# Kernel tuning notes

Hardware: AMD Instinct MI355X
Metric: run time of the kernel (lower is better)

## Reference

```python
import jax, jax.numpy as jnp
from jax import lax
import numpy as np

C = 192      # dim
L = 2        # focal_level
T = 8        # num_frames
KS = (3, 5)  # kernel_size = focal_factor*k + focal_window
B, H, W = 32, 56, 56  # B = 4 clips * T frames


def _gelu(v):
    return jax.nn.gelu(v, approximate=False)  # torch nn.GELU (erf)


def _dwconv2d(x, w):
    # x: (B,C,H,W), w: (C,1,k,k) depthwise; odd k + SAME == padding k//2
    return lax.conv_general_dilated(x, w, (1, 1), 'SAME',
                                    feature_group_count=x.shape[1],
                                    dimension_numbers=('NCHW', 'OIHW', 'NCHW'))


def _conv1d(x, w):
    # x: (N,C,T), w: (Cout,Cin,k) dense conv1d, SAME padding
    return lax.conv_general_dilated(x, w, (1,), 'SAME',
                                    dimension_numbers=('NCH', 'OIH', 'NCH'))


def setup_inputs() -> dict:
    key = jax.random.key(0)
    ks = jax.random.split(key, 12)
    s = 0.02
    return {
        'x':   jax.random.normal(ks[0], (B, H, W, C), jnp.float32),
        'Wf':  jax.random.normal(ks[1], (C, 2 * C + L + 1), jnp.float32) * s,
        'bf':  jnp.zeros((2 * C + L + 1,), jnp.float32),
        'Wft': jax.random.normal(ks[2], (C, C + L + 1), jnp.float32) * s,
        'bft': jnp.zeros((C + L + 1,), jnp.float32),
        'fw0': jax.random.normal(ks[3], (C, 1, KS[0], KS[0]), jnp.float32) * s,
        'fw1': jax.random.normal(ks[4], (C, 1, KS[1], KS[1]), jnp.float32) * s,
        'tw0': jax.random.normal(ks[5], (C, C, KS[0]), jnp.float32) * s,
        'tw1': jax.random.normal(ks[6], (C, C, KS[1]), jnp.float32) * s,
        'Wh':  jax.random.normal(ks[7], (C, C), jnp.float32) * s,
        'bh':  jnp.zeros((C,), jnp.float32),
        'Wht': jax.random.normal(ks[8], (C, C), jnp.float32) * s,
        'bht': jnp.zeros((C,), jnp.float32),
        'Wp':  jax.random.normal(ks[9], (C, C), jnp.float32) * s,
        'bp':  jnp.zeros((C,), jnp.float32),
    }


def reference(x, Wf, bf, Wft, bft, fw0, fw1, tw0, tw1, Wh, bh, Wht, bht, Wp, bp):
    Bt, Hh, Ww, Cc = x.shape
    b = Bt // T
    # ---- temporal branch: (b t) h w c -> (b h w) t c
    xt = x.reshape(b, T, Hh, Ww, Cc).transpose(0, 2, 3, 1, 4).reshape(b * Hh * Ww, T, Cc)
    xt = (xt @ Wft + bft).transpose(0, 2, 1)          # (N, C+L+1, T)
    ctx_t, gates_t = xt[:, :Cc], xt[:, Cc:]
    ctx_all_t = jnp.zeros_like(ctx_t)
    for l, tw in enumerate((tw0, tw1)):
        ctx_t = _gelu(_conv1d(ctx_t, tw))
        ctx_all_t = ctx_all_t + ctx_t * gates_t[:, l:l + 1]
    ctx_all_t = ctx_all_t + _gelu(ctx_t.mean(2, keepdims=True)) * gates_t[:, L:]
    mod_t = jnp.einsum('nct,oc->not', ctx_all_t, Wht) + bht[None, :, None]  # h_temporal 1x1
    # (b h w) c t -> (b t) c h w
    mod_t = mod_t.reshape(b, Hh, Ww, Cc, T).transpose(0, 4, 3, 1, 2).reshape(Bt, Cc, Hh, Ww)
    # ---- spatial branch
    xs = (x @ Wf + bf).transpose(0, 3, 1, 2)           # (B, 2C+L+1, H, W)
    q, ctx, gates = xs[:, :Cc], xs[:, Cc:2 * Cc], xs[:, 2 * Cc:]
    ctx_all = jnp.zeros_like(ctx)
    for l, fw in enumerate((fw0, fw1)):
        ctx = _gelu(_dwconv2d(ctx, fw))
        ctx_all = ctx_all + ctx * gates[:, l:l + 1]
    ctx_all = ctx_all + _gelu(ctx.mean((2, 3), keepdims=True)) * gates[:, L:]
    mod = jnp.einsum('bchw,oc->bohw', ctx_all, Wh) + bh[None, :, None, None]  # h 1x1
    x_out = (q * mod * mod_t).transpose(0, 2, 3, 1)    # (B,H,W,C)
    return x_out @ Wp + bp
```

## Files before the change

### kernel.cpp

```cpp
#include <hip/hip_runtime.h>
#include <math.h>

#define CC    192
#define TT    8
#define HH    56
#define WWD   56
#define PP    3136
#define NTOK  100352
#define NSEQ  12544

typedef __attribute__((ext_vector_type(8))) short short8v;
typedef __attribute__((ext_vector_type(4))) float f32x4;
using u16 = unsigned short;

__device__ __forceinline__ float gelu_f(float v) {
  return 0.5f * v * (1.0f + erff(v * 0.70710678f));
}

__device__ __forceinline__ u16 bf16hi(float f) {
  unsigned u = __builtin_bit_cast(unsigned, f);
  u += 0x7fffu + ((u >> 16) & 1u);
  return (u16)(u >> 16);
}
__device__ __forceinline__ float bf2f(u16 h) {
  unsigned u = ((unsigned)h) << 16;
  return __builtin_bit_cast(float, u);
}

__device__ __forceinline__ void split4(float4 v, uint2* ph, uint2* pl) {
  float vv[4] = {v.x, v.y, v.z, v.w};
  u16 hh[4], ll[4];
  #pragma unroll
  for (int u = 0; u < 4; ++u) {
    hh[u] = bf16hi(vv[u]);
    ll[u] = bf16hi(vv[u] - bf2f(hh[u]));
  }
  *ph = make_uint2((unsigned)hh[0] | ((unsigned)hh[1] << 16),
                   (unsigned)hh[2] | ((unsigned)hh[3] << 16));
  *pl = make_uint2((unsigned)ll[0] | ((unsigned)ll[1] << 16),
                   (unsigned)ll[2] | ((unsigned)ll[3] << 16));
}

__global__ __launch_bounds__(256) void k_wsplit(const float* __restrict__ in,
    u16* __restrict__ hi, u16* __restrict__ lo, int K) {
  int idx = blockIdx.x * 256 + threadIdx.x;
  int total = CC * CC * K;
  if (idx >= total) return;
  int i = idx % CC;
  int rest = idx / CC;
  int o = rest % CC;
  int k = rest / CC;
  float f = in[(o * CC + i) * K + k];
  u16 h = bf16hi(f);
  hi[idx] = h;
  lo[idx] = bf16hi(f - bf2f(h));
}

__global__ __launch_bounds__(256) void k_wsplit_in(const float* __restrict__ Wf,
    const float* __restrict__ Wft, u16* __restrict__ hi, u16* __restrict__ lo) {
  int idx = blockIdx.x * 256 + threadIdx.x;
  if (idx >= 768 * CC) return;
  int k = idx % CC;
  int j = idx / CC;
  float f = 0.0f;
  if (j < 387) f = Wf[k * 387 + j];
  else if (j < 582) f = Wft[k * 195 + (j - 387)];
  u16 h = bf16hi(f);
  hi[idx] = h;
  lo[idx] = bf16hi(f - bf2f(h));
}

__global__ __launch_bounds__(256) void k_wsplit_d(const float* __restrict__ in,
    u16* __restrict__ hi, u16* __restrict__ lo) {
  int idx = blockIdx.x * 256 + threadIdx.x;
  if (idx >= CC * CC) return;
  float f = in[idx];
  u16 h = bf16hi(f);
  hi[idx] = h;
  lo[idx] = bf16hi(f - bf2f(h));
}

__global__ __launch_bounds__(256) void k_wsplit_t(const float* __restrict__ in,
    u16* __restrict__ hi, u16* __restrict__ lo) {
  int idx = blockIdx.x * 256 + threadIdx.x;
  if (idx >= CC * CC) return;
  int c = idx % CC;
  int o = idx / CC;
  float f = in[c * CC + o];
  u16 h = bf16hi(f);
  hi[idx] = h;
  lo[idx] = bf16hi(f - bf2f(h));
}

__global__ __launch_bounds__(256, 3) void k_in_mfma(const float* __restrict__ x,
    const u16* __restrict__ WIh, const u16* __restrict__ WIl,
    const float* __restrict__ bf, const float* __restrict__ bft,
    float* __restrict__ QS, float* __restrict__ CS, float* __restrict__ GS,
    float* __restrict__ CT, float* __restrict__ GT)
{
  __shared__ __align__(16) u16 xh[32 * 200];
  __shared__ __align__(16) u16 xl[32 * 200];
  const int tid  = threadIdx.x;
  const int lane = tid & 63;
  const int w    = tid >> 6;
  const int lrow = lane & 15;
  const int lk   = (lane >> 4) * 8;
  const int orow = (lane >> 4) * 4;
  const int tk0  = blockIdx.x * 32;
  const int jw0  = blockIdx.y * 320 + w * 80;

  #pragma unroll
  for (int it = 0; it < 6; ++it) {
    int idx = tid + it * 256;
    int tokl = idx / 48;
    int c = (idx - tokl * 48) * 4;
    float4 v = *(const float4*)(x + (size_t)(tk0 + tokl) * CC + c);
    split4(v, (uint2*)&xh[tokl * 200 + c], (uint2*)&xl[tokl * 200 + c]);
  }
  __syncthreads();

  f32x4 acc[5][2] = {};
  #pragma unroll
  for (int kb = 0; kb < 6; ++kb) {
    int k0 = kb * 32;
    short8v ah[5], al[5], bh[2], bl[2];
    #pragma unroll
    for (int r = 0; r < 5; ++r) {
      size_t aoff = (size_t)(jw0 + r * 16 + lrow) * 192 + k0 + lk;
      ah[r] = *(const short8v*)(WIh + aoff);
      al[r] = *(const short8v*)(WIl + aoff);
    }
    #pragma unroll
    for (int c = 0; c < 2; ++c) {
      int tokl = c * 16 + lrow;
      bh[c] = *(const short8v*)&xh[tokl * 200 + k0 + lk];
      bl[c] = *(const short8v*)&xl[tokl * 200 + k0 + lk];
    }
    #pragma unroll
    for (int r = 0; r < 5; ++r)
      #pragma unroll
      for (int c = 0; c < 2; ++c) {
        acc[r][c] = __builtin_amdgcn_mfma_f32_16x16x32_bf16(ah[r], bh[c], acc[r][c], 0, 0, 0);
        acc[r][c] = __builtin_amdgcn_mfma_f32_16x16x32_bf16(ah[r], bl[c], acc[r][c], 0, 0, 0);
        acc[r][c] = __builtin_amdgcn_mfma_f32_16x16x32_bf16(al[r], bh[c], acc[r][c], 0, 0, 0);
      }
  }

  #pragma unroll
  for (int c = 0; c < 2; ++c) {
    int tok = tk0 + c * 16 + lrow;
    int bb = tok / PP;
    int hw = tok - bb * PP;
    size_t ctbase = ((size_t)((bb >> 3) * PP + hw) * 8 + (size_t)(bb & 7));
    #pragma unroll
    for (int r = 0; r < 5; ++r) {
      int jb = jw0 + r * 16 + orow;
      #pragma unroll
      for (int u = 0; u < 4; ++u) {
        int j = jb + u;
        if (j >= 582) continue;
        float bias = (j < 387) ? bf[j] : bft[j - 387];
        float val = acc[r][c][u] + bias;
        if (j < 192)      QS[(size_t)tok * CC + j] = val;
        else if (j < 384) CS[(size_t)tok * CC + (j - 192)] = val;
        else if (j < 387) GS[(size_t)tok * 3 + (j - 384)] = val;
        else if (j < 579) CT[ctbase * CC + (j - 387)] = val;
        else              GT[ctbase * 3 + (j - 579)] = val;
      }
    }
  }
}

#define PADB 200
__global__ __launch_bounds__(256, 3) void k_t_mfma(
    const float* __restrict__ CT, const float* __restrict__ GT,
    const u16* __restrict__ W3h,
    const u16* __restrict__ W5h,
    const u16* __restrict__ WHh, const u16* __restrict__ WHl,
    const float* __restrict__ bht, float* __restrict__ MT)
{
  __shared__ __align__(16) u16 bufh[48 * PADB];
  __shared__ __align__(16) u16 bufl[48 * PADB];
  __shared__ float gbuf[96];

  const int tid  = threadIdx.x;
  const int lane = tid & 63;
  const int w    = tid >> 6;
  const int m0   = w * 48;
  const int lrow = lane & 15;
  const int lk   = (lane >> 4) * 8;
  const int orow = (lane >> 4) * 4;
  const int n0   = blockIdx.x * 4;

  if (tid < 96) gbuf[tid] = GT[(size_t)n0 * 24 + tid];

  for (int i = tid; i < 16 * 96; i += 256) {
    int hc = i / 96, j = i - hc * 96;
    int s = hc >> 2, which = hc & 3;
    int pc = s * 12 + ((which < 2) ? which : (8 + which));
    ((unsigned*)&bufh[pc * PADB])[j] = 0u;
    ((unsigned*)&bufl[pc * PADB])[j] = 0u;
  }

  {
    const float4* src = (const float4*)(CT + (size_t)n0 * 1536);
    #pragma unroll
    for (int it = 0; it < 6; ++it) {
      int idx = tid + it * 256;
      int e = idx * 4;
      int s = e / 1536;
      int r2 = e - s * 1536;
      int t = r2 / 192;
      int c = r2 - t * 192;
      float4 v = src[idx];
      int pc = s * 12 + 2 + t;
      split4(v, (uint2*)&bufh[pc * PADB + c], (uint2*)&bufl[pc * PADB + c]);
    }
  }
  __syncthreads();

  int pcolBase[2];
  #pragma unroll
  for (int c = 0; c < 2; ++c) {
    int col = c * 16 + lrow;
    pcolBase[c] = (col >> 3) * 12 + 2 + (col & 7);
  }

#define LOADA1(WH, OFF, KB, AH) { \
    _Pragma("unroll") for (int r = 0; r < 3; ++r) { \
      size_t aoff = ((size_t)((OFF) * 192 + m0 + r * 16 + lrow)) * 192 + (KB) * 32 + lk; \
      AH[r] = *(const short8v*)(WH + aoff); } }
#define LOADB_T(SH, KB, BH, BL) { \
    _Pragma("unroll") for (int c = 0; c < 2; ++c) { \
      int pc = pcolBase[c] + (SH); \
      BH[c] = *(const short8v*)&bufh[pc * PADB + (KB) * 32 + lk]; \
      BL[c] = *(const short8v*)&bufl[pc * PADB + (KB) * 32 + lk]; } }
#define MFMA4(AH, BH, BL, ACC) { \
    _Pragma("unroll") for (int r = 0; r < 3; ++r) \
      _Pragma("unroll") for (int c = 0; c < 2; ++c) { \
        ACC[r][c] = __builtin_amdgcn_mfma_f32_16x16x32_bf16(AH[r], BH[c], ACC[r][c], 0, 0, 0); \
        ACC[r][c] = __builtin_amdgcn_mfma_f32_16x16x32_bf16(AH[r], BL[c], ACC[r][c], 0, 0, 0); } }

  f32x4 acc[3][2] = {};
  #pragma unroll
  for (int off = 0; off < 3; ++off) {
    #pragma unroll
    for (int kb = 0; kb < 6; ++kb) {
      short8v ah[3], bh[2], bl[2];
      LOADA1(W3h, off, kb, ah);
      LOADB_T(off - 1, kb, bh, bl);
      MFMA4(ah, bh, bl, acc);
    }
  }
  __syncthreads();

  #pragma unroll
  for (int r = 0; r < 3; ++r) {
    int o = m0 + r * 16 + orow;
    #pragma unroll
    for (int c = 0; c < 2; ++c) {
      int pc = pcolBase[c];
      f32x4 a = acc[r][c];
      u16 hh[4], ll[4];
      #pragma unroll
      for (int u = 0; u < 4; ++u) {
        float c1v = gelu_f(a[u]);
        hh[u] = bf16hi(c1v);
        ll[u] = bf16hi(c1v - bf2f(hh[u]));
      }
      *(uint2*)&bufh[pc * PADB + o] =
          make_uint2((unsigned)hh[0] | ((unsigned)hh[1] << 16),
                     (unsigned)hh[2] | ((unsigned)hh[3] << 16));
      *(uint2*)&bufl[pc * PADB + o] =
          make_uint2((unsigned)ll[0] | ((unsigned)ll[1] << 16),
                     (unsigned)ll[2] | ((unsigned)ll[3] << 16));
    }
  }
  __syncthreads();

  f32x4 acc2[3][2] = {};
  #pragma unroll
  for (int off = 0; off < 5; ++off) {
    #pragma unroll
    for (int kb = 0; kb < 6; ++kb) {
      short8v ah[3], bh[2], bl[2];
      LOADA1(W5h, off, kb, ah);
      LOADB_T(off - 2, kb, bh, bl);
      MFMA4(ah, bh, bl, acc2);
    }
  }
  __syncthreads();

  #pragma unroll
  for (int r = 0; r < 3; ++r) {
    int o = m0 + r * 16 + orow;
    #pragma unroll
    for (int c = 0; c < 2; ++c) {
      int col = c * 16 + lrow;
      int pc = pcolBase[c];
      float g0 = gbuf[col * 3 + 0];
      float g1 = gbuf[col * 3 + 1];
      float g2 = gbuf[col * 3 + 2];
      f32x4 a = acc2[r][c];
      uint2 c1hv = *(const uint2*)&bufh[pc * PADB + o];
      uint2 c1lv = *(const uint2*)&bufl[pc * PADB + o];
      u16 c1h4[4] = {(u16)(c1hv.x & 0xffff), (u16)(c1hv.x >> 16),
                     (u16)(c1hv.y & 0xffff), (u16)(c1hv.y >> 16)};
      u16 c1l4[4] = {(u16)(c1lv.x & 0xffff), (u16)(c1lv.x >> 16),
                     (u16)(c1lv.y & 0xffff), (u16)(c1lv.y >> 16)};
      u16 hh[4], ll[4];
      #pragma unroll
      for (int u = 0; u < 4; ++u) {
        float cv = gelu_f(a[u]);
        float sm = cv;
        sm += __shfl_xor(sm, 1);
        sm += __shfl_xor(sm, 2);
        sm += __shfl_xor(sm, 4);
        float gm = gelu_f(sm * 0.125f);
        float c1full = bf2f(c1h4[u]) + bf2f(c1l4[u]);
        float av = c1full * g0 + cv * g1 + gm * g2;
        hh[u] = bf16hi(av);
        ll[u] = bf16hi(av - bf2f(hh[u]));
      }
      *(uint2*)&bufh[pc * PADB + o] =
          make_uint2((unsigned)hh[0] | ((unsigned)hh[1] << 16),
                     (unsigned)hh[2] | ((unsigned)hh[3] << 16));
      *(uint2*)&bufl[pc * PADB + o] =
          make_uint2((unsigned)ll[0] | ((unsigned)ll[1] << 16),
                     (unsigned)ll[2] | ((unsigned)ll[3] << 16));
    }
  }
  __syncthreads();

  f32x4 acc3[3][2] = {};
  #pragma unroll
  for (int kb = 0; kb < 6; ++kb) {
    short8v ah[3], al[3], bh[2], bl[2];
    #pragma unroll
    for (int r = 0; r < 3; ++r) {
      size_t aoff = ((size_t)(m0 + r * 16 + lrow)) * 192 + kb * 32 + lk;
      ah[r] = *(const short8v*)(WHh + aoff);
      al[r] = *(const short8v*)(WHl + aoff);
    }
    LOADB_T(0, kb, bh, bl);
    #pragma unroll
    for (int r = 0; r < 3; ++r)
      #pragma unroll
      for (int c = 0; c < 2; ++c) {
        acc3[r][c] = __builtin_amdgcn_mfma_f32_16x16x32_bf16(ah[r], bh[c], acc3[r][c], 0, 0, 0);
        acc3[r][c] = __builtin_amdgcn_mfma_f32_16x16x32_bf16(ah[r], bl[c], acc3[r][c], 0, 0, 0);
        acc3[r][c] = __builtin_amdgcn_mfma_f32_16x16x32_bf16(al[r], bh[c], acc3[r][c], 0, 0, 0);
      }
  }
#undef LOADA1
#undef LOADB_T
#undef MFMA4

  #pragma unroll
  for (int r = 0; r < 3; ++r) {
    int o = m0 + r * 16 + orow;
    float4 bb4 = *(const float4*)&bht[o];
    #pragma unroll
    for (int c = 0; c < 2; ++c) {
      int col = c * 16 + lrow;
      int n = n0 + (col >> 3);
      int t = col & 7;
      int bg = n / PP;
      int hw = n - bg * PP;
      size_t tk = (size_t)(bg * 8 + t) * PP + hw;
      f32x4 a = acc3[r][c];
      *(float4*)&MT[tk * CC + o] =
          make_float4(a[0] + bb4.x, a[1] + bb4.y, a[2] + bb4.z, a[3] + bb4.w);
    }
  }
}

__global__ __launch_bounds__(256) void k_dwf(const float* __restrict__ CTX,
    const float* __restrict__ GS, const float* __restrict__ fw0,
    const float* __restrict__ fw1, float* __restrict__ A0,
    float* __restrict__ GMpart)
{
  __shared__ __align__(16) float sctx[14 * 14 * 32];
  __shared__ __align__(16) float sc1[12 * 12 * 32];
  __shared__ float w3s[9 * 32];
  __shared__ float w5s[25 * 32];
  __shared__ float smean[256];
  const int tid  = threadIdx.x;
  const int tile = blockIdx.x;
  const int cgi  = blockIdx.y;
  const int bb   = blockIdx.z;
  const int ty0  = (tile / 7) * 8;
  const int tx0  = (tile % 7) * 8;
  const int c0   = cgi * 32;

  for (int i = tid; i < 288; i += 256) {
    int k = i / 32, c = i - (i / 32) * 32;
    w3s[k * 32 + c] = fw0[(c0 + c) * 9 + k];
  }
  for (int i = tid; i < 800; i += 256) {
    int k = i / 32, c = i - (i / 32) * 32;
    w5s[k * 32 + c] = fw1[(c0 + c) * 25 + k];
  }

  for (int i = tid; i < 1568; i += 256) {
    int tok = i >> 3;
    int part = i & 7;
    int y = tok / 14, x = tok - y * 14;
    int gh = ty0 + y - 3, gw = tx0 + x - 3;
    float4 v = make_float4(0.f, 0.f, 0.f, 0.f);
    if (gh >= 0 && gh < HH && gw >= 0 && gw < WWD)
      v = *(const float4*)(CTX + ((size_t)bb * PP + gh * WWD + gw) * CC + c0 + part * 4);
    *(float4*)&sctx[tok * 32 + part * 4] = v;
  }
  __syncthreads();

  for (int i = tid; i < 4608; i += 256) {
    int c = i & 31, tok = i >> 5;
    int y = tok / 12, x = tok - y * 12;
    float s = 0.f;
    #pragma unroll
    for (int dy = 0; dy < 3; ++dy)
      #pragma unroll
      for (int dx = 0; dx < 3; ++dx)
        s = fmaf(sctx[((y + dy) * 14 + (x + dx)) * 32 + c], w3s[(dy * 3 + dx) * 32 + c], s);
    sc1[tok * 32 + c] = gelu_f(s);
  }
  __syncthreads();

  float ms = 0.f;
  #pragma unroll
  for (int p = 0; p < 8; ++p) {
    int i = tid + p * 256;
    int c = i & 31, tok = i >> 5;
    int y = tok >> 3, x = tok & 7;
    float s = 0.f;
    #pragma unroll
    for (int dy = 0; dy < 5; ++dy)
      #pragma unroll
      for (int dx = 0; dx < 5; ++dx)
        s = fmaf(sc1[((y + dy) * 12 + (x + dx)) * 32 + c], w5s[(dy * 5 + dx) * 32 + c], s);
    float c2 = gelu_f(s);
    ms += c2;
    float c1v = sc1[((y + 2) * 12 + (x + 2)) * 32 + c];
    size_t tg = (size_t)bb * PP + (size_t)(ty0 + y) * WWD + (tx0 + x);
    float g0 = GS[tg * 3 + 0];
    float g1 = GS[tg * 3 + 1];
    A0[tg * CC + c0 + c] = c1v * g0 + c2 * g1;
  }
  smean[tid] = ms;
  __syncthreads();
  if (tid < 32) {
    float s = 0.f;
    #pragma unroll
    for (int p = 0; p < 8; ++p) s += smean[p * 32 + tid];
    GMpart[(size_t)tile * 6144 + bb * CC + c0 + tid] = s;
  }
}

__global__ __launch_bounds__(256) void k_gmg(const float* __restrict__ GMpart,
                                             float* __restrict__ GMg)
{
  int i = blockIdx.x * 256 + threadIdx.x;
  if (i >= 6144) return;
  float s = 0.f;
  for (int p = 0; p < 49; ++p) s += GMpart[(size_t)p * 6144 + i];
  GMg[i] = gelu_f(s * (1.0f / 3136.0f));
}

__global__ __launch_bounds__(256, 3) void k_mod_mfma(float* __restrict__ A0MOD,
    const float* __restrict__ GS, const float* __restrict__ GMg,
    const u16* __restrict__ Wmh, const u16* __restrict__ Wml,
    const float* __restrict__ bh)
{
  __shared__ __align__(16) u16 sh_[32 * 200];
  __shared__ __align__(16) u16 sl_[32 * 200];
  const int tid  = threadIdx.x;
  const int lane = tid & 63;
  const int w    = tid >> 6;
  const int lrow = lane & 15;
  const int lk   = (lane >> 4) * 8;
  const int orow = (lane >> 4) * 4;
  const int tk0  = blockIdx.x * 32;
  const int m0   = w * 48;

  #pragma unroll
  for (int it = 0; it < 6; ++it) {
    int idx = tid + it * 256;
    int tokl = idx / 48;
    int c = (idx - tokl * 48) * 4;
    int tok = tk0 + tokl;
    int bb = tok / PP;
    size_t base = (size_t)tok * CC + c;
    float4 v1 = *(const float4*)(A0MOD + base);
    float4 vg = *(const float4*)(GMg + bb * CC + c);
    float g2 = GS[(size_t)tok * 3 + 2];
    float4 av = make_float4(v1.x + vg.x * g2, v1.y + vg.y * g2,
                            v1.z + vg.z * g2, v1.w + vg.w * g2);
    split4(av, (uint2*)&sh_[tokl * 200 + c], (uint2*)&sl_[tokl * 200 + c]);
  }
  __syncthreads();

  f32x4 acc[3][2] = {};
  #pragma unroll
  for (int kb = 0; kb < 6; ++kb) {
    int k0 = kb * 32;
    short8v ah[3], al[3], bh4[2], bl4[2];
    #pragma unroll
    for (int r = 0; r < 3; ++r) {
      size_t aoff = (size_t)(m0 + r * 16 + lrow) * 192 + k0 + lk;
      ah[r] = *(const short8v*)(Wmh + aoff);
      al[r] = *(const short8v*)(Wml + aoff);
    }
    #pragma unroll
    for (int c = 0; c < 2; ++c) {
      int tokl = c * 16 + lrow;
      bh4[c] = *(const short8v*)&sh_[tokl * 200 + k0 + lk];
      bl4[c] = *(const short8v*)&sl_[tokl * 200 + k0 + lk];
    }
    #pragma unroll
    for (int r = 0; r < 3; ++r)
      #pragma unroll
      for (int c = 0; c < 2; ++c) {
        acc[r][c] = __builtin_amdgcn_mfma_f32_16x16x32_bf16(ah[r], bh4[c], acc[r][c], 0, 0, 0);
        acc[r][c] = __builtin_amdgcn_mfma_f32_16x16x32_bf16(ah[r], bl4[c], acc[r][c], 0, 0, 0);
        acc[r][c] = __builtin_amdgcn_mfma_f32_16x16x32_bf16(al[r], bh4[c], acc[r][c], 0, 0, 0);
      }
  }
  __syncthreads();

  #pragma unroll
  for (int r = 0; r < 3; ++r) {
    int jb = m0 + r * 16 + orow;
    float4 b4 = *(const float4*)&bh[jb];
    #pragma unroll
    for (int c = 0; c < 2; ++c) {
      int tok = tk0 + c * 16 + lrow;
      f32x4 a = acc[r][c];
      *(float4*)&A0MOD[(size_t)tok * CC + jb] =
          make_float4(a[0] + b4.x, a[1] + b4.y, a[2] + b4.z, a[3] + b4.w);
    }
  }
}

__global__ __launch_bounds__(256, 3) void k_out_mfma(const float* __restrict__ QS,
    const float* __restrict__ MOD, float* MTout,
    const u16* __restrict__ Wph, const u16* __restrict__ Wpl,
    const float* __restrict__ bp)
{
  __shared__ __align__(16) u16 sh_[32 * 200];
  __shared__ __align__(16) u16 sl_[32 * 200];
  const int tid  = threadIdx.x;
  const int lane = tid & 63;
  const int w    = tid >> 6;
  const int lrow = lane & 15;
  const int lk   = (lane >> 4) * 8;
  const int orow = (lane >> 4) * 4;
  const int tk0  = blockIdx.x * 32;
  const int m0   = w * 48;

  #pragma unroll
  for (int it = 0; it < 6; ++it) {
    int idx = tid + it * 256;
    int tokl = idx / 48;
    int c = (idx - tokl * 48) * 4;
    size_t base = (size_t)(tk0 + tokl) * CC + c;
    float4 q  = *(const float4*)(QS + base);
    float4 md = *(const float4*)(MOD + base);
    float4 mt = *(const float4*)(MTout + base);
    float4 av = make_float4(q.x * md.x * mt.x, q.y * md.y * mt.y,
                            q.z * md.z * mt.z, q.w * md.w * mt.w);
    split4(av, (uint2*)&sh_[tokl * 200 + c], (uint2*)&sl_[tokl * 200 + c]);
  }
  __syncthreads();

  f32x4 acc[3][2] = {};
  #pragma unroll
  for (int kb = 0; kb < 6; ++kb) {
    int k0 = kb * 32;
    short8v ah[3], al[3], bh4[2], bl4[2];
    #pragma unroll
    for (int r = 0; r < 3; ++r) {
      size_t aoff = (size_t)(m0 + r * 16 + lrow) * 192 + k0 + lk;
      ah[r] = *(const short8v*)(Wph + aoff);
      al[r] = *(const short8v*)(Wpl + aoff);
    }
    #pragma unroll
    for (int c = 0; c < 2; ++c) {
      int tokl = c * 16 + lrow;
      bh4[c] = *(const short8v*)&sh_[tokl * 200 + k0 + lk];
      bl4[c] = *(const short8v*)&sl_[tokl * 200 + k0 + lk];
    }
    #pragma unroll
    for (int r = 0; r < 3; ++r)
      #pragma unroll
      for (int c = 0; c < 2; ++c) {
        acc[r][c] = __builtin_amdgcn_mfma_f32_16x16x32_bf16(ah[r], bh4[c], acc[r][c], 0, 0, 0);
        acc[r][c] = __builtin_amdgcn_mfma_f32_16x16x32_bf16(ah[r], bl4[c], acc[r][c], 0, 0, 0);
        acc[r][c] = __builtin_amdgcn_mfma_f32_16x16x32_bf16(al[r], bh4[c], acc[r][c], 0, 0, 0);
      }
  }
  __syncthreads();

  #pragma unroll
  for (int r = 0; r < 3; ++r) {
    int jb = m0 + r * 16 + orow;
    float4 b4 = *(const float4*)&bp[jb];
    #pragma unroll
    for (int c = 0; c < 2; ++c) {
      int tok = tk0 + c * 16 + lrow;
      f32x4 a = acc[r][c];
      *(float4*)&MTout[(size_t)tok * CC + jb] =
          make_float4(a[0] + b4.x, a[1] + b4.y, a[2] + b4.z, a[3] + b4.w);
    }
  }
}

extern "C" void kernel_launch(void* const* d_in, const int* in_sizes, int n_in,
                              void* d_out, int out_size, void* d_ws, size_t ws_size,
                              hipStream_t stream)
{
  (void)in_sizes; (void)n_in; (void)out_size; (void)ws_size;
  const float* x   = (const float*)d_in[0];
  const float* Wf  = (const float*)d_in[1];
  const float* bf  = (const float*)d_in[2];
  const float* Wft = (const float*)d_in[3];
  const float* bft = (const float*)d_in[4];
  const float* fw0 = (const float*)d_in[5];
  const float* fw1 = (const float*)d_in[6];
  const float* tw0 = (const float*)d_in[7];
  const float* tw1 = (const float*)d_in[8];
  const float* Wh  = (const float*)d_in[9];
  const float* bh  = (const float*)d_in[10];
  const float* Wht = (const float*)d_in[11];
  const float* bht = (const float*)d_in[12];
  const float* Wp  = (const float*)d_in[13];
  const float* bp  = (const float*)d_in[14];

  float* ws = (float*)d_ws;
  const size_t SZ = (size_t)NTOK * CC;
  float* QS     = ws + 0 * SZ;
  float* WS1    = ws + 1 * SZ;
  float* WS2    = ws + 2 * SZ;
  float* MT     = (float*)d_out;
  float* GS     = ws + 3 * SZ;
  float* GT     = GS + (size_t)NTOK * 3;
  float* GMpart = GT + (size_t)NTOK * 3;
  float* GMg    = GMpart + 49 * 6144;
  u16* W3h = (u16*)(GMg + 6144);
  u16* W3l = W3h + 3 * 36864;
  u16* W5h = W3l + 3 * 36864;
  u16* W5l = W5h + 5 * 36864;
  u16* WHh = W5l + 5 * 36864;
  u16* WHl = WHh + 36864;
  u16* WIh = WHl + 36864;
  u16* WIl = WIh + 768 * 192;
  u16* Wmh = WIl + 768 * 192;
  u16* Wml = Wmh + 36864;
  u16* Wph = Wml + 36864;
  u16* Wpl = Wph + 36864;

  k_wsplit<<<432, 256, 0, stream>>>(tw0, W3h, W3l, 3);
  k_wsplit<<<720, 256, 0, stream>>>(tw1, W5h, W5l, 5);
  k_wsplit<<<144, 256, 0, stream>>>(Wht, WHh, WHl, 1);
  k_wsplit_in<<<576, 256, 0, stream>>>(Wf, Wft, WIh, WIl);
  k_wsplit_d<<<144, 256, 0, stream>>>(Wh, Wmh, Wml);
  k_wsplit_t<<<144, 256, 0, stream>>>(Wp, Wph, Wpl);

  k_in_mfma<<<dim3(3136, 2), 256, 0, stream>>>(x, WIh, WIl, bf, bft,
                                               QS, WS1, GS, WS2, GT);
  k_t_mfma<<<3136, 256, 0, stream>>>(WS2, GT, W3h, W5h, WHh, WHl, bht, MT);

  k_dwf<<<dim3(49, 6, 32), 256, 0, stream>>>(WS1, GS, fw0, fw1, WS2, GMpart);
  k_gmg<<<24, 256, 0, stream>>>(GMpart, GMg);

  k_mod_mfma<<<3136, 256, 0, stream>>>(WS2, GS, GMg, Wmh, Wml, bh);
  k_out_mfma<<<3136, 256, 0, stream>>>(QS, WS2, MT, Wph, Wpl, bp);
}
```

Baseline: 973.5 us.

## Fuse modulation and output projection kernels; halve temporal kernel tile per block

The h-projection GEMM and the output projection GEMM now run in one kernel. The modulator is kept in shared memory as a bf16 hi/lo split instead of being written to and re-read from global memory. Separately, the temporal conv kernel now handles 2 sequences per block instead of 4, doubling the grid, halving LDS use and raising launch bounds to 4 blocks per SM for occupancy. The cost is that each weight fragment loaded from global memory is reused across fewer columns in the temporal kernel.

```diff
diff --git a/kernel.cpp b/kernel.cpp
--- a/kernel.cpp
+++ b/kernel.cpp
@@ -172,16 +172,16 @@
 }
 
 #define PADB 200
-__global__ __launch_bounds__(256, 3) void k_t_mfma(
+__global__ __launch_bounds__(256, 4) void k_t_mfma(
     const float* __restrict__ CT, const float* __restrict__ GT,
     const u16* __restrict__ W3h,
     const u16* __restrict__ W5h,
     const u16* __restrict__ WHh, const u16* __restrict__ WHl,
     const float* __restrict__ bht, float* __restrict__ MT)
 {
-  __shared__ __align__(16) u16 bufh[48 * PADB];
-  __shared__ __align__(16) u16 bufl[48 * PADB];
-  __shared__ float gbuf[96];
+  __shared__ __align__(16) u16 bufh[24 * PADB];
+  __shared__ __align__(16) u16 bufl[24 * PADB];
+  __shared__ float gbuf[48];
 
   const int tid  = threadIdx.x;
   const int lane = tid & 63;
@@ -190,11 +190,11 @@
   const int lrow = lane & 15;
   const int lk   = (lane >> 4) * 8;
   const int orow = (lane >> 4) * 4;
-  const int n0   = blockIdx.x * 4;
-
-  if (tid < 96) gbuf[tid] = GT[(size_t)n0 * 24 + tid];
-
-  for (int i = tid; i < 16 * 96; i += 256) {
+  const int n0   = blockIdx.x * 2;
+
+  if (tid < 48) gbuf[tid] = GT[(size_t)n0 * 24 + tid];
+
+  for (int i = tid; i < 8 * 96; i += 256) {
     int hc = i / 96, j = i - hc * 96;
     int s = hc >> 2, which = hc & 3;
     int pc = s * 12 + ((which < 2) ? which : (8 + which));
@@ -205,7 +205,7 @@
   {
     const float4* src = (const float4*)(CT + (size_t)n0 * 1536);
     #pragma unroll
-    for (int it = 0; it < 6; ++it) {
+    for (int it = 0; it < 3; ++it) {
       int idx = tid + it * 256;
       int e = idx * 4;
       int s = e / 1536;
@@ -219,37 +219,30 @@
   }
   __syncthreads();
 
-  int pcolBase[2];
-  #pragma unroll
-  for (int c = 0; c < 2; ++c) {
-    int col = c * 16 + lrow;
-    pcolBase[c] = (col >> 3) * 12 + 2 + (col & 7);
-  }
+  const int pcb = (lrow >> 3) * 12 + 2 + (lrow & 7);
 
 #define LOADA1(WH, OFF, KB, AH) { \
     _Pragma("unroll") for (int r = 0; r < 3; ++r) { \
       size_t aoff = ((size_t)((OFF) * 192 + m0 + r * 16 + lrow)) * 192 + (KB) * 32 + lk; \
       AH[r] = *(const short8v*)(WH + aoff); } }
-#define LOADB_T(SH, KB, BH, BL) { \
-    _Pragma("unroll") for (int c = 0; c < 2; ++c) { \
-      int pc = pcolBase[c] + (SH); \
-      BH[c] = *(const short8v*)&bufh[pc * PADB + (KB) * 32 + lk]; \
-      BL[c] = *(const short8v*)&bufl[pc * PADB + (KB) * 32 + lk]; } }
-#define MFMA4(AH, BH, BL, ACC) { \
-    _Pragma("unroll") for (int r = 0; r < 3; ++r) \
-      _Pragma("unroll") for (int c = 0; c < 2; ++c) { \
-        ACC[r][c] = __builtin_amdgcn_mfma_f32_16x16x32_bf16(AH[r], BH[c], ACC[r][c], 0, 0, 0); \
-        ACC[r][c] = __builtin_amdgcn_mfma_f32_16x16x32_bf16(AH[r], BL[c], ACC[r][c], 0, 0, 0); } }
-
-  f32x4 acc[3][2] = {};
+#define LOADB1(SH, KB, BH, BL) { \
+    int pc = pcb + (SH); \
+    BH = *(const short8v*)&bufh[pc * PADB + (KB) * 32 + lk]; \
+    BL = *(const short8v*)&bufl[pc * PADB + (KB) * 32 + lk]; }
+#define MFMA2(AH, BH, BL, ACC) { \
+    _Pragma("unroll") for (int r = 0; r < 3; ++r) { \
+      ACC[r] = __builtin_amdgcn_mfma_f32_16x16x32_bf16(AH[r], BH, ACC[r], 0, 0, 0); \
+      ACC[r] = __builtin_amdgcn_mfma_f32_16x16x32_bf16(AH[r], BL, ACC[r], 0, 0, 0); } }
+
+  f32x4 acc[3] = {};
   #pragma unroll
   for (int off = 0; off < 3; ++off) {
     #pragma unroll
     for (int kb = 0; kb < 6; ++kb) {
-      short8v ah[3], bh[2], bl[2];
+      short8v ah[3], bh, bl;
       LOADA1(W3h, off, kb, ah);
-      LOADB_T(off - 1, kb, bh, bl);
-      MFMA4(ah, bh, bl, acc);
+      LOADB1(off - 1, kb, bh, bl);
+      MFMA2(ah, bh, bl, acc);
     }
   }
   __syncthreads();
@@ -257,53 +250,46 @@
   #pragma unroll
   for (int r = 0; r < 3; ++r) {
     int o = m0 + r * 16 + orow;
-    #pragma unroll
-    for (int c = 0; c < 2; ++c) {
-      int pc = pcolBase[c];
-      f32x4 a = acc[r][c];
-      u16 hh[4], ll[4];
-      #pragma unroll
-      for (int u = 0; u < 4; ++u) {
-        float c1v = gelu_f(a[u]);
-        hh[u] = bf16hi(c1v);
-        ll[u] = bf16hi(c1v - bf2f(hh[u]));
-      }
-      *(uint2*)&bufh[pc * PADB + o] =
-          make_uint2((unsigned)hh[0] | ((unsigned)hh[1] << 16),
-                     (unsigned)hh[2] | ((unsigned)hh[3] << 16));
-      *(uint2*)&bufl[pc * PADB + o] =
-          make_uint2((unsigned)ll[0] | ((unsigned)ll[1] << 16),
-                     (unsigned)ll[2] | ((unsigned)ll[3] << 16));
-    }
-  }
-  __syncthreads();
-
-  f32x4 acc2[3][2] = {};
+    f32x4 a = acc[r];
+    u16 hh[4], ll[4];
+    #pragma unroll
+    for (int u = 0; u < 4; ++u) {
+      float c1v = gelu_f(a[u]);
+      hh[u] = bf16hi(c1v);
+      ll[u] = bf16hi(c1v - bf2f(hh[u]));
+    }
+    *(uint2*)&bufh[pcb * PADB + o] =
+        make_uint2((unsigned)hh[0] | ((unsigned)hh[1] << 16),
+                   (unsigned)hh[2] | ((unsigned)hh[3] << 16));
+    *(uint2*)&bufl[pcb * PADB + o] =
+        make_uint2((unsigned)ll[0] | ((unsigned)ll[1] << 16),
+                   (unsigned)ll[2] | ((unsigned)ll[3] << 16));
+  }
+  __syncthreads();
+
+  f32x4 acc2[3] = {};
   #pragma unroll
   for (int off = 0; off < 5; ++off) {
     #pragma unroll
     for (int kb = 0; kb < 6; ++kb) {
-      short8v ah[3], bh[2], bl[2];
+      short8v ah[3], bh, bl;
       LOADA1(W5h, off, kb, ah);
-      LOADB_T(off - 2, kb, bh, bl);
-      MFMA4(ah, bh, bl, acc2);
-    }
-  }
-  __syncthreads();
-
-  #pragma unroll
-  for (int r = 0; r < 3; ++r) {
-    int o = m0 + r * 16 + orow;
-    #pragma unroll
-    for (int c = 0; c < 2; ++c) {
-      int col = c * 16 + lrow;
-      int pc = pcolBase[c];
-      float g0 = gbuf[col * 3 + 0];
-      float g1 = gbuf[col * 3 + 1];
-      float g2 = gbuf[col * 3 + 2];
-      f32x4 a = acc2[r][c];
-      uint2 c1hv = *(const uint2*)&bufh[pc * PADB + o];
-      uint2 c1lv = *(const uint2*)&bufl[pc * PADB + o];
+      LOADB1(off - 2, kb, bh, bl);
+      MFMA2(ah, bh, bl, acc2);
+    }
+  }
+  __syncthreads();
+
+  {
+    float g0 = gbuf[lrow * 3 + 0];
+    float g1 = gbuf[lrow * 3 + 1];
+    float g2 = gbuf[lrow * 3 + 2];
+    #pragma unroll
+    for (int r = 0; r < 3; ++r) {
+      int o = m0 + r * 16 + orow;
+      f32x4 a = acc2[r];
+      uint2 c1hv = *(const uint2*)&bufh[pcb * PADB + o];
+      uint2 c1lv = *(const uint2*)&bufl[pcb * PADB + o];
       u16 c1h4[4] = {(u16)(c1hv.x & 0xffff), (u16)(c1hv.x >> 16),
                      (u16)(c1hv.y & 0xffff), (u16)(c1hv.y >> 16)};
       u16 c1l4[4] = {(u16)(c1lv.x & 0xffff), (u16)(c1lv.x >> 16),
@@ -322,53 +308,49 @@
         hh[u] = bf16hi(av);
         ll[u] = bf16hi(av - bf2f(hh[u]));
       }
-      *(uint2*)&bufh[pc * PADB + o] =
+      *(uint2*)&bufh[pcb * PADB + o] =
           make_uint2((unsigned)hh[0] | ((unsigned)hh[1] << 16),
                      (unsigned)hh[2] | ((unsigned)hh[3] << 16));
-      *(uint2*)&bufl[pc * PADB + o] =
+      *(uint2*)&bufl[pcb * PADB + o] =
           make_uint2((unsigned)ll[0] | ((unsigned)ll[1] << 16),
                      (unsigned)ll[2] | ((unsigned)ll[3] << 16));
     }
   }
   __syncthreads();
 
-  f32x4 acc3[3][2] = {};
+  f32x4 acc3[3] = {};
   #pragma unroll
   for (int kb = 0; kb < 6; ++kb) {
-    short8v ah[3], al[3], bh[2], bl[2];
+    short8v ah[3], al[3], bh, bl;
     #pragma unroll
     for (int r = 0; r < 3; ++r) {
       size_t aoff = ((size_t)(m0 + r * 16 + lrow)) * 192 + kb * 32 + lk;
       ah[r] = *(const short8v*)(WHh + aoff);
       al[r] = *(const short8v*)(WHl + aoff);
     }
-    LOADB_T(0, kb, bh, bl);
-    #pragma unroll
-    for (int r = 0; r < 3; ++r)
-      #pragma unroll
-      for (int c = 0; c < 2; ++c) {
-        acc3[r][c] = __builtin_amdgcn_mfma_f32_16x16x32_bf16(ah[r], bh[c], acc3[r][c], 0, 0, 0);
-        acc3[r][c] = __builtin_amdgcn_mfma_f32_16x16x32_bf16(ah[r], bl[c], acc3[r][c], 0, 0, 0);
-        acc3[r][c] = __builtin_amdgcn_mfma_f32_16x16x32_bf16(al[r], bh[c], acc3[r][c], 0, 0, 0);
-      }
+    LOADB1(0, kb, bh, bl);
+    #pragma unroll
+    for (int r = 0; r < 3; ++r) {
+      acc3[r] = __builtin_amdgcn_mfma_f32_16x16x32_bf16(ah[r], bh, acc3[r], 0, 0, 0);
+      acc3[r] = __builtin_amdgcn_mfma_f32_16x16x32_bf16(ah[r], bl, acc3[r], 0, 0, 0);
+      acc3[r] = __builtin_amdgcn_mfma_f32_16x16x32_bf16(al[r], bh, acc3[r], 0, 0, 0);
+    }
   }
 #undef LOADA1
-#undef LOADB_T
-#undef MFMA4
-
-  #pragma unroll
-  for (int r = 0; r < 3; ++r) {
-    int o = m0 + r * 16 + orow;
-    float4 bb4 = *(const float4*)&bht[o];
-    #pragma unroll
-    for (int c = 0; c < 2; ++c) {
-      int col = c * 16 + lrow;
-      int n = n0 + (col >> 3);
-      int t = col & 7;
-      int bg = n / PP;
-      int hw = n - bg * PP;
-      size_t tk = (size_t)(bg * 8 + t) * PP + hw;
-      f32x4 a = acc3[r][c];
+#undef LOADB1
+#undef MFMA2
+
+  {
+    int n = n0 + (lrow >> 3);
+    int t = lrow & 7;
+    int bg = n / PP;
+    int hw = n - bg * PP;
+    size_t tk = (size_t)(bg * 8 + t) * PP + hw;
+    #pragma unroll
+    for (int r = 0; r < 3; ++r) {
+      int o = m0 + r * 16 + orow;
+      float4 bb4 = *(const float4*)&bht[o];
+      f32x4 a = acc3[r];
       *(float4*)&MT[tk * CC + o] =
           make_float4(a[0] + bb4.x, a[1] + bb4.y, a[2] + bb4.z, a[3] + bb4.w);
     }
@@ -467,84 +449,11 @@
   GMg[i] = gelu_f(s * (1.0f / 3136.0f));
 }
 
-__global__ __launch_bounds__(256, 3) void k_mod_mfma(float* __restrict__ A0MOD,
+__global__ __launch_bounds__(256, 3) void k_modout(float* __restrict__ A0,
     const float* __restrict__ GS, const float* __restrict__ GMg,
     const u16* __restrict__ Wmh, const u16* __restrict__ Wml,
-    const float* __restrict__ bh)
-{
-  __shared__ __align__(16) u16 sh_[32 * 200];
-  __shared__ __align__(16) u16 sl_[32 * 200];
-  const int tid  = threadIdx.x;
-  const int lane = tid & 63;
-  const int w    = tid >> 6;
-  const int lrow = lane & 15;
-  const int lk   = (lane >> 4) * 8;
-  const int orow = (lane >> 4) * 4;
-  const int tk0  = blockIdx.x * 32;
-  const int m0   = w * 48;
-
-  #pragma unroll
-  for (int it = 0; it < 6; ++it) {
-    int idx = tid + it * 256;
-    int tokl = idx / 48;
-    int c = (idx - tokl * 48) * 4;
-    int tok = tk0 + tokl;
-    int bb = tok / PP;
-    size_t base = (size_t)tok * CC + c;
-    float4 v1 = *(const float4*)(A0MOD + base);
-    float4 vg = *(const float4*)(GMg + bb * CC + c);
-    float g2 = GS[(size_t)tok * 3 + 2];
-    float4 av = make_float4(v1.x + vg.x * g2, v1.y + vg.y * g2,
-                            v1.z + vg.z * g2, v1.w + vg.w * g2);
-    split4(av, (uint2*)&sh_[tokl * 200 + c], (uint2*)&sl_[tokl * 200 + c]);
-  }
-  __syncthreads();
-
-  f32x4 acc[3][2] = {};
-  #pragma unroll
-  for (int kb = 0; kb < 6; ++kb) {
-    int k0 = kb * 32;
-    short8v ah[3], al[3], bh4[2], bl4[2];
-    #pragma unroll
-    for (int r = 0; r < 3; ++r) {
-      size_t aoff = (size_t)(m0 + r * 16 + lrow) * 192 + k0 + lk;
-      ah[r] = *(const short8v*)(Wmh + aoff);
-      al[r] = *(const short8v*)(Wml + aoff);
-    }
-    #pragma unroll
-    for (int c = 0; c < 2; ++c) {
-      int tokl = c * 16 + lrow;
-      bh4[c] = *(const short8v*)&sh_[tokl * 200 + k0 + lk];
-      bl4[c] = *(const short8v*)&sl_[tokl * 200 + k0 + lk];
-    }
-    #pragma unroll
-    for (int r = 0; r < 3; ++r)
-      #pragma unroll
-      for (int c = 0; c < 2; ++c) {
-        acc[r][c] = __builtin_amdgcn_mfma_f32_16x16x32_bf16(ah[r], bh4[c], acc[r][c], 0, 0, 0);
-        acc[r][c] = __builtin_amdgcn_mfma_f32_16x16x32_bf16(ah[r], bl4[c], acc[r][c], 0, 0, 0);
-        acc[r][c] = __builtin_amdgcn_mfma_f32_16x16x32_bf16(al[r], bh4[c], acc[r][c], 0, 0, 0);
-      }
-  }
-  __syncthreads();
-
-  #pragma unroll
-  for (int r = 0; r < 3; ++r) {
-    int jb = m0 + r * 16 + orow;
-    float4 b4 = *(const float4*)&bh[jb];
-    #pragma unroll
-    for (int c = 0; c < 2; ++c) {
-      int tok = tk0 + c * 16 + lrow;
-      f32x4 a = acc[r][c];
-      *(float4*)&A0MOD[(size_t)tok * CC + jb] =
-          make_float4(a[0] + b4.x, a[1] + b4.y, a[2] + b4.z, a[3] + b4.w);
-    }
-  }
-}
-
-__global__ __launch_bounds__(256, 3) void k_out_mfma(const float* __restrict__ QS,
-    const float* __restrict__ MOD, float* MTout,
-    const u16* __restrict__ Wph, const u16* __restrict__ Wpl,
+    const float* __restrict__ bh, const float* __restrict__ QS,
+    float* MTout, const u16* __restrict__ Wph, const u16* __restrict__ Wpl,
     const float* __restrict__ bp)
 {
   __shared__ __align__(16) u16 sh_[32 * 200];
@@ -563,43 +472,82 @@
     int idx = tid + it * 256;
     int tokl = idx / 48;
     int c = (idx - tokl * 48) * 4;
+    int tok = tk0 + tokl;
+    int bb = tok / PP;
+    size_t base = (size_t)tok * CC + c;
+    float4 v1 = *(const float4*)(A0 + base);
+    float4 vg = *(const float4*)(GMg + bb * CC + c);
+    float g2 = GS[(size_t)tok * 3 + 2];
+    float4 av = make_float4(v1.x + vg.x * g2, v1.y + vg.y * g2,
+                            v1.z + vg.z * g2, v1.w + vg.w * g2);
+    split4(av, (uint2*)&sh_[tokl * 200 + c], (uint2*)&sl_[tokl * 200 + c]);
+  }
+  __syncthreads();
+
+#define LOADA_G(WH, WL, KB, AH, AL) { \
+    _Pragma("unroll") for (int r = 0; r < 3; ++r) { \
+      size_t aoff = (size_t)(m0 + r * 16 + lrow) * 192 + (KB) * 32 + lk; \
+      AH[r] = *(const short8v*)(WH + aoff); \
+      AL[r] = *(const short8v*)(WL + aoff); } }
+#define LOADB_G(KB, BH, BL) { \
+    _Pragma("unroll") for (int c = 0; c < 2; ++c) { \
+      int tokl = c * 16 + lrow; \
+      BH[c] = *(const short8v*)&sh_[tokl * 200 + (KB) * 32 + lk]; \
+      BL[c] = *(const short8v*)&sl_[tokl * 200 + (KB) * 32 + lk]; } }
+#define GEMM6(WH, WL, ACC) { \
+    _Pragma("unroll") for (int kb = 0; kb < 6; ++kb) { \
+      short8v ah[3], al[3], bh4[2], bl4[2]; \
+      LOADA_G(WH, WL, kb, ah, al); \
+      LOADB_G(kb, bh4, bl4); \
+      _Pragma("unroll") for (int r = 0; r < 3; ++r) \
+        _Pragma("unroll") for (int c = 0; c < 2; ++c) { \
+          ACC[r][c] = __builtin_amdgcn_mfma_f32_16x16x32_bf16(ah[r], bh4[c], ACC[r][c], 0, 0, 0); \
+          ACC[r][c] = __builtin_amdgcn_mfma_f32_16x16x32_bf16(ah[r], bl4[c], ACC[r][c], 0, 0, 0); \
+          ACC[r][c] = __builtin_amdgcn_mfma_f32_16x16x32_bf16(al[r], bh4[c], ACC[r][c], 0, 0, 0); } } }
+
+  f32x4 acc[3][2] = {};
+  GEMM6(Wmh, Wml, acc);
+  __syncthreads();
+
+  #pragma unroll
+  for (int r = 0; r < 3; ++r) {
+    int jb = m0 + r * 16 + orow;
+    float4 b4 = *(const float4*)&bh[jb];
+    #pragma unroll
+    for (int c = 0; c < 2; ++c) {
+      int tokl = c * 16 + lrow;
+      f32x4 a = acc[r][c];
+      float4 mv = make_float4(a[0] + b4.x, a[1] + b4.y, a[2] + b4.z, a[3] + b4.w);
+      split4(mv, (uint2*)&sh_[tokl * 200 + jb], (uint2*)&sl_[tokl * 200 + jb]);
+    }
+  }
+  __syncthreads();
+
+  #pragma unroll
+  for (int it = 0; it < 6; ++it) {
+    int idx = tid + it * 256;
+    int tokl = idx / 48;
+    int c = (idx - tokl * 48) * 4;
     size_t base = (size_t)(tk0 + tokl) * CC + c;
     float4 q  = *(const float4*)(QS + base);
-    float4 md = *(const float4*)(MOD + base);
     float4 mt = *(const float4*)(MTout + base);
-    float4 av = make_float4(q.x * md.x * mt.x, q.y * md.y * mt.y,
-                            q.z * md.z * mt.z, q.w * md.w * mt.w);
+    uint2 mh = *(const uint2*)&sh_[tokl * 200 + c];
+    uint2 ml = *(const uint2*)&sl_[tokl * 200 + c];
+    float m0v = bf2f((u16)(mh.x & 0xffff)) + bf2f((u16)(ml.x & 0xffff));
+    float m1v = bf2f((u16)(mh.x >> 16))    + bf2f((u16)(ml.x >> 16));
+    float m2v = bf2f((u16)(mh.y & 0xffff)) + bf2f((u16)(ml.y & 0xffff));
+    float m3v = bf2f((u16)(mh.y >> 16))    + bf2f((u16)(ml.y >> 16));
+    float4 av = make_float4(q.x * m0v * mt.x, q.y * m1v * mt.y,
+                            q.z * m2v * mt.z, q.w * m3v * mt.w);
     split4(av, (uint2*)&sh_[tokl * 200 + c], (uint2*)&sl_[tokl * 200 + c]);
   }
   __syncthreads();
 
-  f32x4 acc[3][2] = {};
-  #pragma unroll
-  for (int kb = 0; kb < 6; ++kb) {
-    int k0 = kb * 32;
-    short8v ah[3], al[3], bh4[2], bl4[2];
-    #pragma unroll
-    for (int r = 0; r < 3; ++r) {
-      size_t aoff = (size_t)(m0 + r * 16 + lrow) * 192 + k0 + lk;
-      ah[r] = *(const short8v*)(Wph + aoff);
-      al[r] = *(const short8v*)(Wpl + aoff);
-    }
-    #pragma unroll
-    for (int c = 0; c < 2; ++c) {
-      int tokl = c * 16 + lrow;
-      bh4[c] = *(const short8v*)&sh_[tokl * 200 + k0 + lk];
-      bl4[c] = *(const short8v*)&sl_[tokl * 200 + k0 + lk];
-    }
-    #pragma unroll
-    for (int r = 0; r < 3; ++r)
-      #pragma unroll
-      for (int c = 0; c < 2; ++c) {
-        acc[r][c] = __builtin_amdgcn_mfma_f32_16x16x32_bf16(ah[r], bh4[c], acc[r][c], 0, 0, 0);
-        acc[r][c] = __builtin_amdgcn_mfma_f32_16x16x32_bf16(ah[r], bl4[c], acc[r][c], 0, 0, 0);
-        acc[r][c] = __builtin_amdgcn_mfma_f32_16x16x32_bf16(al[r], bh4[c], acc[r][c], 0, 0, 0);
-      }
-  }
-  __syncthreads();
+  f32x4 acc2[3][2] = {};
+  GEMM6(Wph, Wpl, acc2);
+#undef LOADA_G
+#undef LOADB_G
+#undef GEMM6
 
   #pragma unroll
   for (int r = 0; r < 3; ++r) {
@@ -608,7 +556,7 @@
     #pragma unroll
     for (int c = 0; c < 2; ++c) {
       int tok = tk0 + c * 16 + lrow;
-      f32x4 a = acc[r][c];
+      f32x4 a = acc2[r][c];
       *(float4*)&MTout[(size_t)tok * CC + jb] =
           make_float4(a[0] + b4.x, a[1] + b4.y, a[2] + b4.z, a[3] + b4.w);
     }
@@ -668,11 +616,11 @@
 
   k_in_mfma<<<dim3(3136, 2), 256, 0, stream>>>(x, WIh, WIl, bf, bft,
                                                QS, WS1, GS, WS2, GT);
-  k_t_mfma<<<3136, 256, 0, stream>>>(WS2, GT, W3h, W5h, WHh, WHl, bht, MT);
+  k_t_mfma<<<6272, 256, 0, stream>>>(WS2, GT, W3h, W5h, WHh, WHl, bht, MT);
 
   k_dwf<<<dim3(49, 6, 32), 256, 0, stream>>>(WS1, GS, fw0, fw1, WS2, GMpart);
   k_gmg<<<24, 256, 0, stream>>>(GMpart, GMg);
 
-  k_mod_mfma<<<3136, 256, 0, stream>>>(WS2, GS, GMg, Wmh, Wml, bh);
-  k_out_mfma<<<3136, 256, 0, stream>>>(QS, WS2, MT, Wph, Wpl, bp);
-}
+  k_modout<<<3136, 256, 0, stream>>>(WS2, GS, GMg, Wmh, Wml, bh,
+                                     QS, MT, Wph, Wpl, bp);
+}
```

Result: slower. 1.180 ms (+21.2%).
